# Optimization experiments

Measured on AMD Instinct MI355X. Metric: run time of the kernel, lower is better.

Reference implementation:

```python
import jax, jax.numpy as jnp
import numpy as np
from jax import lax

B, CIN, COUT, WDIM, K, H, W_ = 8, 512, 512, 512, 3, 64, 64

def setup_inputs() -> dict:
    key = jax.random.key(0)
    ks = jax.random.split(key, 7)
    x = jax.random.normal(ks[0], (B, CIN, H, W_), dtype=jnp.float32)
    w = jax.random.normal(ks[1], (B, WDIM), dtype=jnp.float32)
    noise = jax.random.normal(ks[2], (B, COUT, H, W_), dtype=jnp.float32)
    # params (kaiming-ish scale for weight; demodulation normalizes anyway)
    weight = jax.random.normal(ks[3], (1, COUT, CIN, K, K), dtype=jnp.float32) * 0.05
    affine_w = jax.random.normal(ks[4], (CIN, WDIM), dtype=jnp.float32) * (1.0 / np.sqrt(WDIM))
    affine_b = jnp.zeros((CIN,), dtype=jnp.float32)
    bias = jnp.zeros((COUT,), dtype=jnp.float32)
    return {"x": x, "w": w, "noise": noise, "weight": weight,
            "affine_w": affine_w, "affine_b": affine_b, "bias": bias}

def reference(x, w, noise, weight, affine_w, affine_b, bias):
    b, cin, h, ww = x.shape
    cout, k = weight.shape[1], weight.shape[3]
    # style: affine(w) + 1
    s = jnp.einsum('bd,cd->bc', w, affine_w) + affine_b          # [B, Cin]
    s = s[:, None, :, None, None] + 1.0                           # [B,1,Cin,1,1]
    w_mod = weight * s                                            # [B,Cout,Cin,k,k]
    d = lax.rsqrt(jnp.sum(w_mod * w_mod, axis=(2, 3, 4), keepdims=True) + 1e-8)
    w_mod = w_mod * d
    # grouped conv: groups = B
    x_ = x.reshape(1, b * cin, h, ww)
    w_ = w_mod.reshape(b * cout, cin, k, k)
    pad = k // 2
    y = lax.conv_general_dilated(
        x_, w_, window_strides=(1, 1), padding=[(pad, pad), (pad, pad)],
        feature_group_count=b,
        dimension_numbers=('NCHW', 'OIHW', 'NCHW'))
    y = y.reshape(b, cout, h, ww)
    y = y + noise + bias[None, :, None, None]
    return jnp.where(y >= 0, y, 0.2 * y)
```

## Files before the change

kernel.cpp:

```cpp
#include <hip/hip_runtime.h>
#include <hip/hip_bf16.h>


#define CIN   512
#define COUT  512
#define KDIM  4608
#define HWPIX 4096

typedef __attribute__((ext_vector_type(8))) __bf16 bf16x8;
typedef __attribute__((ext_vector_type(4))) float  f32x4;

__device__ __forceinline__ unsigned short f2bf(float f){
  union { float f; unsigned int u; } v; v.f = f;
  unsigned int u = v.u;
  u += 0x7fffu + ((u >> 16) & 1u);
  return (unsigned short)(u >> 16);
}

#define GLDS16(g, l) __builtin_amdgcn_global_load_lds(                      \
    (const __attribute__((address_space(1))) unsigned int*)(g),             \
    (__attribute__((address_space(3))) unsigned int*)(l), 16, 0, 0)

__global__ void style_k(const float* __restrict__ w, const float* __restrict__ aw,
                        const float* __restrict__ ab, float* __restrict__ styles){
  int wid = threadIdx.x >> 6, lane = threadIdx.x & 63;
  int gid = blockIdx.x * 4 + wid;
  int b = gid >> 9, c = gid & 511;
  const float* wb = w + b * 512;
  const float* ar = aw + c * 512;
  float sum = 0.f;
  for (int j = lane; j < 512; j += 64) sum += wb[j] * ar[j];
  for (int off = 32; off; off >>= 1) sum += __shfl_down(sum, off, 64);
  if (lane == 0) styles[gid] = sum + ab[c] + 1.0f;
}

__global__ void modw_k(const float* __restrict__ weight, const float* __restrict__ styles,
                       unsigned short* __restrict__ wmod){
  int o = blockIdx.x, b = blockIdx.y;
  int t = threadIdx.x;
  const float* wrow = weight + (size_t)o * KDIM;
  const float* st   = styles + b * 512;
  __shared__ unsigned short sw[9 * 520];
  __shared__ float red[4];
  float vals[18];
  float part = 0.f;
#pragma unroll
  for (int it = 0; it < 18; ++it){
    int idx = it * 256 + t;
    int i = idx / 9;
    float v = wrow[idx] * st[i];
    vals[it] = v;
    part += v * v;
  }
  int wid = t >> 6, lane = t & 63;
  for (int off = 32; off; off >>= 1) part += __shfl_down(part, off, 64);
  if (lane == 0) red[wid] = part;
  __syncthreads();
  float d = rsqrtf(red[0] + red[1] + red[2] + red[3] + 1e-8f);
#pragma unroll
  for (int it = 0; it < 18; ++it){
    int idx = it * 256 + t;
    int i = idx / 9;
    int tap = idx - i * 9;
    sw[tap * 520 + i] = f2bf(vals[it] * d);
  }
  __syncthreads();
  unsigned int* orow32 = (unsigned int*)(wmod + ((size_t)(b * 512 + o)) * KDIM);
#pragma unroll
  for (int it = 0; it < 9; ++it){
    int u = it * 256 + t;
    int e = u * 2;
    int tap2 = e >> 9, i2 = e & 511;
    orow32[u] = *(const unsigned int*)&sw[tap2 * 520 + i2];
  }
}

__global__ void xpose_k(const float* __restrict__ x, unsigned short* __restrict__ xpad){
  int h = blockIdx.x, cg = blockIdx.y, b = blockIdx.z;
  int c0 = cg * 64;
  __shared__ unsigned short lds[64][66];
  int t = threadIdx.x;
  const float* xb = x + (((size_t)(b * 512 + c0)) * 64 + h) * 64;
#pragma unroll
  for (int it = 0; it < 16; ++it){
    int idx = it * 256 + t;
    int cl = idx >> 6, wl = idx & 63;
    lds[wl][cl] = f2bf(xb[(size_t)cl * 4096 + wl]);
  }
  __syncthreads();
#pragma unroll
  for (int it = 0; it < 2; ++it){
    int idx = it * 256 + t;
    int wl = idx >> 3, ch = idx & 7;
    unsigned int u0 = *(const unsigned int*)&lds[wl][ch * 8 + 0];
    unsigned int u1 = *(const unsigned int*)&lds[wl][ch * 8 + 2];
    unsigned int u2 = *(const unsigned int*)&lds[wl][ch * 8 + 4];
    unsigned int u3 = *(const unsigned int*)&lds[wl][ch * 8 + 6];
    int off = ((b * 66 + h + 1) * 66 + (wl + 1)) * 512 + c0 + ch * 8;
    *(uint4*)&xpad[off] = make_uint4(u0, u1, u2, u3);
  }
}

__global__ __launch_bounds__(256, 4) void conv_gemm(
    const unsigned short* __restrict__ wmod, const unsigned short* __restrict__ xpad,
    const float* __restrict__ noise, const float* __restrict__ bias,
    float* __restrict__ out){
  __shared__ unsigned short As[2][128 * 32];
  __shared__ unsigned short Bs[2][128 * 32];
  int g = blockIdx.x;
  int xcd = g & 7, sl = g >> 3;
  int grp = xcd * 4 + (sl >> 5);
  int nt  = sl & 31;
  int b = grp >> 2, mt = grp & 3;
  int m0 = mt * 128, n0 = nt * 128;
  int h0 = n0 >> 6;
  int tid = threadIdx.x, wid = tid >> 6, lane = tid & 63;
  int wm = wid >> 1, wn = wid & 1;
  int lr = lane >> 2;
  int lc = lane & 3;

  const unsigned short* wbase = wmod + ((size_t)(b * 512 + m0)) * KDIM;
  int aoff0 = ((wid * 2 + 0) * 16 + lr) * KDIM + lc * 8;
  int aoff1 = ((wid * 2 + 1) * 16 + lr) * KDIM + lc * 8;

  const unsigned short* xb = xpad + (size_t)b * 66 * 66 * 512;
  int p0 = (wid * 2 + 0) * 16 + lr;
  int p1 = (wid * 2 + 1) * 16 + lr;
  int boff0 = ((h0 + (p0 >> 6) + 1) * 66 + ((p0 & 63) + 1)) * 512 + lc * 8;
  int boff1 = ((h0 + (p1 >> 6) + 1) * 66 + ((p1 & 63) + 1)) * 512 + lc * 8;

  int lbase0 = (wid * 2 + 0) * 512;
  int lbase1 = (wid * 2 + 1) * 512;

  int fm = lane & 15;
  int k8 = (lane >> 4) * 8;
  int apo[4], bpo[4];
#pragma unroll
  for (int i = 0; i < 4; ++i){
    apo[i] = (wm * 64 + i * 16 + fm) * 32 + k8;
    bpo[i] = (wn * 64 + i * 16 + fm) * 32 + k8;
  }

  f32x4 acc[4][4];
#pragma unroll
  for (int i = 0; i < 4; ++i)
#pragma unroll
    for (int j = 0; j < 4; ++j) acc[i][j] = (f32x4){0.f, 0.f, 0.f, 0.f};

  for (int ks = 0; ks < 72; ++ks){
    int tap = ks >> 3;
    int c0  = (ks & 7) << 6;
    int k0  = (tap << 9) + c0;
    int dy3 = tap / 3;
    int bshift = (((dy3 - 1) * 66 + (tap - dy3 * 3 - 1)) << 9) + c0;
    __syncthreads();
    GLDS16(wbase + aoff0 + k0,      &As[0][lbase0]);
    GLDS16(wbase + aoff1 + k0,      &As[0][lbase1]);
    GLDS16(wbase + aoff0 + k0 + 32, &As[1][lbase0]);
    GLDS16(wbase + aoff1 + k0 + 32, &As[1][lbase1]);
    GLDS16(xb + boff0 + bshift,      &Bs[0][lbase0]);
    GLDS16(xb + boff1 + bshift,      &Bs[0][lbase1]);
    GLDS16(xb + boff0 + bshift + 32, &Bs[1][lbase0]);
    GLDS16(xb + boff1 + bshift + 32, &Bs[1][lbase1]);
    __syncthreads();
#pragma unroll
    for (int s = 0; s < 2; ++s){
      bf16x8 af[4], bfr[4];
#pragma unroll
      for (int i = 0; i < 4; ++i) af[i]  = *(const bf16x8*)&As[s][apo[i]];
#pragma unroll
      for (int i = 0; i < 4; ++i) bfr[i] = *(const bf16x8*)&Bs[s][bpo[i]];
#pragma unroll
      for (int i = 0; i < 4; ++i)
#pragma unroll
        for (int j = 0; j < 4; ++j)
          acc[i][j] = __builtin_amdgcn_mfma_f32_16x16x32_bf16(af[i], bfr[j], acc[i][j], 0, 0, 0);
    }
  }

  int quad = lane >> 4;
#pragma unroll
  for (int i = 0; i < 4; ++i){
    int o_base = m0 + wm * 64 + i * 16 + quad * 4;
#pragma unroll
    for (int j = 0; j < 4; ++j){
      int n = n0 + wn * 64 + j * 16 + fm;
#pragma unroll
      for (int r = 0; r < 4; ++r){
        int o = o_base + r;
        size_t idx = ((size_t)(b * 512 + o)) * HWPIX + n;
        float v = acc[i][j][r] + noise[idx] + bias[o];
        out[idx] = (v >= 0.f) ? v : 0.2f * v;
      }
    }
  }
}

extern "C" void kernel_launch(void* const* d_in, const int* in_sizes, int n_in,
                              void* d_out, int out_size, void* d_ws, size_t ws_size,
                              hipStream_t stream) {
  const float* x        = (const float*)d_in[0];
  const float* w        = (const float*)d_in[1];
  const float* noise    = (const float*)d_in[2];
  const float* weight   = (const float*)d_in[3];
  const float* affine_w = (const float*)d_in[4];
  const float* affine_b = (const float*)d_in[5];
  const float* bias     = (const float*)d_in[6];
  float* out = (float*)d_out;

  float* styles = (float*)d_ws;
  unsigned short* wmod = (unsigned short*)((char*)d_ws + 16384);
  unsigned short* xpad = (unsigned short*)((char*)d_ws + 16384 + 37748736ull);

  hipMemsetAsync(xpad, 0, 35684352ull, stream);
  style_k<<<dim3(1024), 256, 0, stream>>>(w, affine_w, affine_b, styles);
  modw_k <<<dim3(512, 8), 256, 0, stream>>>(weight, styles, wmod);
  xpose_k<<<dim3(64, 8, 8), 256, 0, stream>>>(x, xpad);
  conv_gemm<<<dim3(1024), 256, 0, stream>>>(wmod, xpad, noise, bias, out);
}
```

Baseline: 362.5 us.

## Double-buffer LDS tiles to prefetch the next K-slice during MFMA compute

The conv GEMM main loop becomes a two-stage software pipeline. The K-step drops from 64 to 32, so there are 144 iterations instead of 72. Each iteration issues global-to-LDS loads for the next slice into the alternate buffer, then runs MFMAs on the current buffer, with one barrier per iteration instead of two. This aims to hide global load latency behind compute, at the cost of twice as many iterations and barriers and less MFMA work per barrier.

```diff
diff --git a/kernel.cpp b/kernel.cpp
--- a/kernel.cpp
+++ b/kernel.cpp
@@ -147,35 +147,36 @@
 #pragma unroll
     for (int j = 0; j < 4; ++j) acc[i][j] = (f32x4){0.f, 0.f, 0.f, 0.f};
 
-  for (int ks = 0; ks < 72; ++ks){
-    int tap = ks >> 3;
-    int c0  = (ks & 7) << 6;
-    int k0  = (tap << 9) + c0;
-    int dy3 = tap / 3;
-    int bshift = (((dy3 - 1) * 66 + (tap - dy3 * 3 - 1)) << 9) + c0;
+  GLDS16(wbase + aoff0, &As[0][lbase0]);
+  GLDS16(wbase + aoff1, &As[0][lbase1]);
+  GLDS16(xb + boff0 - 67 * 512, &Bs[0][lbase0]);
+  GLDS16(xb + boff1 - 67 * 512, &Bs[0][lbase1]);
+
+  for (int ks = 0; ks < 144; ++ks){
+    int buf = ks & 1, nbuf = buf ^ 1;
     __syncthreads();
-    GLDS16(wbase + aoff0 + k0,      &As[0][lbase0]);
-    GLDS16(wbase + aoff1 + k0,      &As[0][lbase1]);
-    GLDS16(wbase + aoff0 + k0 + 32, &As[1][lbase0]);
-    GLDS16(wbase + aoff1 + k0 + 32, &As[1][lbase1]);
-    GLDS16(xb + boff0 + bshift,      &Bs[0][lbase0]);
-    GLDS16(xb + boff1 + bshift,      &Bs[0][lbase1]);
-    GLDS16(xb + boff0 + bshift + 32, &Bs[1][lbase0]);
-    GLDS16(xb + boff1 + bshift + 32, &Bs[1][lbase1]);
-    __syncthreads();
-#pragma unroll
-    for (int s = 0; s < 2; ++s){
-      bf16x8 af[4], bfr[4];
-#pragma unroll
-      for (int i = 0; i < 4; ++i) af[i]  = *(const bf16x8*)&As[s][apo[i]];
-#pragma unroll
-      for (int i = 0; i < 4; ++i) bfr[i] = *(const bf16x8*)&Bs[s][bpo[i]];
-#pragma unroll
-      for (int i = 0; i < 4; ++i)
-#pragma unroll
-        for (int j = 0; j < 4; ++j)
-          acc[i][j] = __builtin_amdgcn_mfma_f32_16x16x32_bf16(af[i], bfr[j], acc[i][j], 0, 0, 0);
+    if (ks + 1 < 144){
+      int kn  = ks + 1;
+      int tap = kn >> 4;
+      int c0  = (kn & 15) << 5;
+      int k0  = kn << 5;
+      int dy3 = tap / 3;
+      int bshift = ((dy3 - 1) * 66 + (tap - dy3 * 3 - 1)) * 512 + c0;
+      GLDS16(wbase + aoff0 + k0,  &As[nbuf][lbase0]);
+      GLDS16(wbase + aoff1 + k0,  &As[nbuf][lbase1]);
+      GLDS16(xb + boff0 + bshift, &Bs[nbuf][lbase0]);
+      GLDS16(xb + boff1 + bshift, &Bs[nbuf][lbase1]);
     }
+    bf16x8 af[4], bfr[4];
+#pragma unroll
+    for (int i = 0; i < 4; ++i) af[i]  = *(const bf16x8*)&As[buf][apo[i]];
+#pragma unroll
+    for (int i = 0; i < 4; ++i) bfr[i] = *(const bf16x8*)&Bs[buf][bpo[i]];
+#pragma unroll
+    for (int i = 0; i < 4; ++i)
+#pragma unroll
+      for (int j = 0; j < 4; ++j)
+        acc[i][j] = __builtin_amdgcn_mfma_f32_16x16x32_bf16(af[i], bfr[j], acc[i][j], 0, 0, 0);
   }
 
   int quad = lane >> 4;
```

Result: slower. 373.9 us (+3.1%).

## Switch GEMM to 32x32x16 MFMA and zero only padding borders in transpose

Applied to the files above, without the earlier changes.

The conv GEMM inner loop now uses 32x32x16 bf16 MFMA with 2x2 accumulator tiles per wave instead of 4x4 tiles of 16x16x32. This halves the number of LDS fragment loads and MFMA issues per k-step, and the epilogue index mapping is updated to the 32x32 output layout. Separately, the full-buffer memset of the padded input is removed and the transpose kernel writes zeros only into the halo rows and columns. The halo writes must cover every border cell, otherwise stale workspace data would enter the convolution.

```diff
diff --git a/kernel.cpp b/kernel.cpp
--- a/kernel.cpp
+++ b/kernel.cpp
@@ -7,8 +7,8 @@
 #define KDIM  4608
 #define HWPIX 4096
 
-typedef __attribute__((ext_vector_type(8))) __bf16 bf16x8;
-typedef __attribute__((ext_vector_type(4))) float  f32x4;
+typedef __attribute__((ext_vector_type(8)))  __bf16 bf16x8;
+typedef __attribute__((ext_vector_type(16))) float  f32x16;
 
 __device__ __forceinline__ unsigned short f2bf(float f){
   union { float f; unsigned int u; } v; v.f = f;
@@ -86,6 +86,19 @@
     int idx = it * 256 + t;
     int cl = idx >> 6, wl = idx & 63;
     lds[wl][cl] = f2bf(xb[(size_t)cl * 4096 + wl]);
+  }
+  if (t < 64){
+    int which = t >> 5;
+    int ch2 = (t & 31) * 2;
+    int wl = which ? 65 : 0;
+    *(unsigned int*)&xpad[(((size_t)b * 66 + h + 1) * 66 + wl) * 512 + c0 + ch2] = 0u;
+  }
+  if (h == 0 || h == 63){
+    int row = (h == 0) ? 0 : 65;
+    for (int u = t; u < 66 * 32; u += 256){
+      int wl = u >> 5, ch2 = (u & 31) * 2;
+      *(unsigned int*)&xpad[(((size_t)b * 66 + row) * 66 + wl) * 512 + c0 + ch2] = 0u;
+    }
   }
   __syncthreads();
 #pragma unroll
@@ -132,20 +145,22 @@
   int lbase0 = (wid * 2 + 0) * 512;
   int lbase1 = (wid * 2 + 1) * 512;
 
-  int fm = lane & 15;
-  int k8 = (lane >> 4) * 8;
-  int apo[4], bpo[4];
-#pragma unroll
-  for (int i = 0; i < 4; ++i){
-    apo[i] = (wm * 64 + i * 16 + fm) * 32 + k8;
-    bpo[i] = (wn * 64 + i * 16 + fm) * 32 + k8;
-  }
-
-  f32x4 acc[4][4];
-#pragma unroll
-  for (int i = 0; i < 4; ++i)
-#pragma unroll
-    for (int j = 0; j < 4; ++j) acc[i][j] = (f32x4){0.f, 0.f, 0.f, 0.f};
+  int ln31 = lane & 31;
+  int hi8  = (lane >> 5) * 8;
+  int apo[2], bpo[2];
+#pragma unroll
+  for (int i = 0; i < 2; ++i){
+    apo[i] = (wm * 64 + i * 32 + ln31) * 32 + hi8;
+    bpo[i] = (wn * 64 + i * 32 + ln31) * 32 + hi8;
+  }
+
+  f32x16 acc[2][2];
+#pragma unroll
+  for (int i = 0; i < 2; ++i)
+#pragma unroll
+    for (int j = 0; j < 2; ++j)
+#pragma unroll
+      for (int r = 0; r < 16; ++r) acc[i][j][r] = 0.f;
 
   for (int ks = 0; ks < 72; ++ks){
     int tap = ks >> 3;
@@ -165,29 +180,32 @@
     __syncthreads();
 #pragma unroll
     for (int s = 0; s < 2; ++s){
-      bf16x8 af[4], bfr[4];
-#pragma unroll
-      for (int i = 0; i < 4; ++i) af[i]  = *(const bf16x8*)&As[s][apo[i]];
-#pragma unroll
-      for (int i = 0; i < 4; ++i) bfr[i] = *(const bf16x8*)&Bs[s][bpo[i]];
-#pragma unroll
-      for (int i = 0; i < 4; ++i)
-#pragma unroll
-        for (int j = 0; j < 4; ++j)
-          acc[i][j] = __builtin_amdgcn_mfma_f32_16x16x32_bf16(af[i], bfr[j], acc[i][j], 0, 0, 0);
+#pragma unroll
+      for (int t = 0; t < 2; ++t){
+        bf16x8 af[2], bfr[2];
+#pragma unroll
+        for (int i = 0; i < 2; ++i) af[i]  = *(const bf16x8*)&As[s][apo[i] + t * 16];
+#pragma unroll
+        for (int i = 0; i < 2; ++i) bfr[i] = *(const bf16x8*)&Bs[s][bpo[i] + t * 16];
+#pragma unroll
+        for (int i = 0; i < 2; ++i)
+#pragma unroll
+          for (int j = 0; j < 2; ++j)
+            acc[i][j] = __builtin_amdgcn_mfma_f32_32x32x16_bf16(af[i], bfr[j], acc[i][j], 0, 0, 0);
+      }
     }
   }
 
-  int quad = lane >> 4;
-#pragma unroll
-  for (int i = 0; i < 4; ++i){
-    int o_base = m0 + wm * 64 + i * 16 + quad * 4;
-#pragma unroll
-    for (int j = 0; j < 4; ++j){
-      int n = n0 + wn * 64 + j * 16 + fm;
-#pragma unroll
-      for (int r = 0; r < 4; ++r){
-        int o = o_base + r;
+  int rbase = (lane >> 5) * 4;
+#pragma unroll
+  for (int i = 0; i < 2; ++i){
+#pragma unroll
+    for (int j = 0; j < 2; ++j){
+      int n = n0 + wn * 64 + j * 32 + ln31;
+#pragma unroll
+      for (int r = 0; r < 16; ++r){
+        int row = (r & 3) + 8 * (r >> 2) + rbase;
+        int o = m0 + wm * 64 + i * 32 + row;
         size_t idx = ((size_t)(b * 512 + o)) * HWPIX + n;
         float v = acc[i][j][r] + noise[idx] + bias[o];
         out[idx] = (v >= 0.f) ? v : 0.2f * v;
@@ -212,7 +230,6 @@
   unsigned short* wmod = (unsigned short*)((char*)d_ws + 16384);
   unsigned short* xpad = (unsigned short*)((char*)d_ws + 16384 + 37748736ull);
 
-  hipMemsetAsync(xpad, 0, 35684352ull, stream);
   style_k<<<dim3(1024), 256, 0, stream>>>(w, affine_w, affine_b, styles);
   modw_k <<<dim3(512, 8), 256, 0, stream>>>(weight, styles, wmod);
   xpose_k<<<dim3(64, 8, 8), 256, 0, stream>>>(x, xpad);
```

After: 396.2 us. 9.3% more time.

## Enlarge GEMM M-tile to 256 and zero only padding borders in transpose

Applied to the files above, without the earlier changes.

The conv GEMM tile grows from 128x128 to 256x128 per block, giving each warp an 8x4 MFMA accumulator grid and halving the grid to 512 blocks. This raises arithmetic intensity per LDS load and cuts redundant loads of the activation tile. The full-buffer memset of the padded input is removed, and the transpose kernel now writes zeros only to the halo rows and columns. The trade-off is doubled accumulator registers and LDS per block, with launch bounds lowered to 2 blocks per SM, which reduces occupancy and may cause register pressure.

```diff
diff --git a/kernel.cpp b/kernel.cpp
--- a/kernel.cpp
+++ b/kernel.cpp
@@ -87,6 +87,19 @@
     int cl = idx >> 6, wl = idx & 63;
     lds[wl][cl] = f2bf(xb[(size_t)cl * 4096 + wl]);
   }
+  if (t < 64){
+    int which = t >> 5;
+    int ch2 = (t & 31) * 2;
+    int wl = which ? 65 : 0;
+    *(unsigned int*)&xpad[(((size_t)b * 66 + h + 1) * 66 + wl) * 512 + c0 + ch2] = 0u;
+  }
+  if (h == 0 || h == 63){
+    int row = (h == 0) ? 0 : 65;
+    for (int u = t; u < 66 * 32; u += 256){
+      int wl = u >> 5, ch2 = (u & 31) * 2;
+      *(unsigned int*)&xpad[(((size_t)b * 66 + row) * 66 + wl) * 512 + c0 + ch2] = 0u;
+    }
+  }
   __syncthreads();
 #pragma unroll
   for (int it = 0; it < 2; ++it){
@@ -101,49 +114,52 @@
   }
 }
 
-__global__ __launch_bounds__(256, 4) void conv_gemm(
+__global__ __launch_bounds__(256, 2) void conv_gemm(
     const unsigned short* __restrict__ wmod, const unsigned short* __restrict__ xpad,
     const float* __restrict__ noise, const float* __restrict__ bias,
     float* __restrict__ out){
-  __shared__ unsigned short As[2][128 * 32];
+  __shared__ unsigned short As[2][256 * 32];
   __shared__ unsigned short Bs[2][128 * 32];
   int g = blockIdx.x;
   int xcd = g & 7, sl = g >> 3;
-  int grp = xcd * 4 + (sl >> 5);
-  int nt  = sl & 31;
-  int b = grp >> 2, mt = grp & 3;
-  int m0 = mt * 128, n0 = nt * 128;
-  int h0 = n0 >> 6;
+  int b = xcd, mt = sl >> 5, nt = sl & 31;
+  int m0 = mt * 256, n0 = nt * 128;
+  int h0 = nt * 2;
   int tid = threadIdx.x, wid = tid >> 6, lane = tid & 63;
   int wm = wid >> 1, wn = wid & 1;
   int lr = lane >> 2;
   int lc = lane & 3;
 
   const unsigned short* wbase = wmod + ((size_t)(b * 512 + m0)) * KDIM;
-  int aoff0 = ((wid * 2 + 0) * 16 + lr) * KDIM + lc * 8;
-  int aoff1 = ((wid * 2 + 1) * 16 + lr) * KDIM + lc * 8;
+  int aoffG[4];
+#pragma unroll
+  for (int i = 0; i < 4; ++i)
+    aoffG[i] = ((wid * 64 + i * 16 + lr)) * KDIM + lc * 8;
 
   const unsigned short* xb = xpad + (size_t)b * 66 * 66 * 512;
-  int p0 = (wid * 2 + 0) * 16 + lr;
-  int p1 = (wid * 2 + 1) * 16 + lr;
-  int boff0 = ((h0 + (p0 >> 6) + 1) * 66 + ((p0 & 63) + 1)) * 512 + lc * 8;
-  int boff1 = ((h0 + (p1 >> 6) + 1) * 66 + ((p1 & 63) + 1)) * 512 + lc * 8;
-
-  int lbase0 = (wid * 2 + 0) * 512;
-  int lbase1 = (wid * 2 + 1) * 512;
+  int boffG[2];
+#pragma unroll
+  for (int i = 0; i < 2; ++i){
+    int p = wid * 32 + i * 16 + lr;
+    boffG[i] = ((h0 + (p >> 6) + 1) * 66 + ((p & 63) + 1)) * 512 + lc * 8;
+  }
+  int albase[4], blbase[2];
+#pragma unroll
+  for (int i = 0; i < 4; ++i) albase[i] = (wid * 64 + i * 16) * 32;
+#pragma unroll
+  for (int i = 0; i < 2; ++i) blbase[i] = (wid * 32 + i * 16) * 32;
 
   int fm = lane & 15;
   int k8 = (lane >> 4) * 8;
-  int apo[4], bpo[4];
-#pragma unroll
-  for (int i = 0; i < 4; ++i){
-    apo[i] = (wm * 64 + i * 16 + fm) * 32 + k8;
-    bpo[i] = (wn * 64 + i * 16 + fm) * 32 + k8;
-  }
-
-  f32x4 acc[4][4];
-#pragma unroll
-  for (int i = 0; i < 4; ++i)
+  int apo[8], bpo[4];
+#pragma unroll
+  for (int i = 0; i < 8; ++i) apo[i] = (wm * 128 + i * 16 + fm) * 32 + k8;
+#pragma unroll
+  for (int j = 0; j < 4; ++j) bpo[j] = (wn * 64 + j * 16 + fm) * 32 + k8;
+
+  f32x4 acc[8][4];
+#pragma unroll
+  for (int i = 0; i < 8; ++i)
 #pragma unroll
     for (int j = 0; j < 4; ++j) acc[i][j] = (f32x4){0.f, 0.f, 0.f, 0.f};
 
@@ -154,24 +170,26 @@
     int dy3 = tap / 3;
     int bshift = (((dy3 - 1) * 66 + (tap - dy3 * 3 - 1)) << 9) + c0;
     __syncthreads();
-    GLDS16(wbase + aoff0 + k0,      &As[0][lbase0]);
-    GLDS16(wbase + aoff1 + k0,      &As[0][lbase1]);
-    GLDS16(wbase + aoff0 + k0 + 32, &As[1][lbase0]);
-    GLDS16(wbase + aoff1 + k0 + 32, &As[1][lbase1]);
-    GLDS16(xb + boff0 + bshift,      &Bs[0][lbase0]);
-    GLDS16(xb + boff1 + bshift,      &Bs[0][lbase1]);
-    GLDS16(xb + boff0 + bshift + 32, &Bs[1][lbase0]);
-    GLDS16(xb + boff1 + bshift + 32, &Bs[1][lbase1]);
+#pragma unroll
+    for (int i = 0; i < 4; ++i){
+      GLDS16(wbase + aoffG[i] + k0,      &As[0][albase[i]]);
+      GLDS16(wbase + aoffG[i] + k0 + 32, &As[1][albase[i]]);
+    }
+#pragma unroll
+    for (int i = 0; i < 2; ++i){
+      GLDS16(xb + boffG[i] + bshift,      &Bs[0][blbase[i]]);
+      GLDS16(xb + boffG[i] + bshift + 32, &Bs[1][blbase[i]]);
+    }
     __syncthreads();
 #pragma unroll
     for (int s = 0; s < 2; ++s){
-      bf16x8 af[4], bfr[4];
-#pragma unroll
-      for (int i = 0; i < 4; ++i) af[i]  = *(const bf16x8*)&As[s][apo[i]];
-#pragma unroll
-      for (int i = 0; i < 4; ++i) bfr[i] = *(const bf16x8*)&Bs[s][bpo[i]];
-#pragma unroll
-      for (int i = 0; i < 4; ++i)
+      bf16x8 af[8], bfr[4];
+#pragma unroll
+      for (int i = 0; i < 8; ++i) af[i]  = *(const bf16x8*)&As[s][apo[i]];
+#pragma unroll
+      for (int j = 0; j < 4; ++j) bfr[j] = *(const bf16x8*)&Bs[s][bpo[j]];
+#pragma unroll
+      for (int i = 0; i < 8; ++i)
 #pragma unroll
         for (int j = 0; j < 4; ++j)
           acc[i][j] = __builtin_amdgcn_mfma_f32_16x16x32_bf16(af[i], bfr[j], acc[i][j], 0, 0, 0);
@@ -180,8 +198,8 @@
 
   int quad = lane >> 4;
 #pragma unroll
-  for (int i = 0; i < 4; ++i){
-    int o_base = m0 + wm * 64 + i * 16 + quad * 4;
+  for (int i = 0; i < 8; ++i){
+    int o_base = m0 + wm * 128 + i * 16 + quad * 4;
 #pragma unroll
     for (int j = 0; j < 4; ++j){
       int n = n0 + wn * 64 + j * 16 + fm;
@@ -212,9 +230,8 @@
   unsigned short* wmod = (unsigned short*)((char*)d_ws + 16384);
   unsigned short* xpad = (unsigned short*)((char*)d_ws + 16384 + 37748736ull);
 
-  hipMemsetAsync(xpad, 0, 35684352ull, stream);
   style_k<<<dim3(1024), 256, 0, stream>>>(w, affine_w, affine_b, styles);
   modw_k <<<dim3(512, 8), 256, 0, stream>>>(weight, styles, wmod);
   xpose_k<<<dim3(64, 8, 8), 256, 0, stream>>>(x, xpad);
-  conv_gemm<<<dim3(1024), 256, 0, stream>>>(wmod, xpad, noise, bias, out);
-}
+  conv_gemm<<<dim3(512), 256, 0, stream>>>(wmod, xpad, noise, bias, out);
+}
```

Measured after the change: 336.9 us. 1.08x faster.
